# Optimization experiments

Hardware: AMD Instinct MI355X
Metric: run time of the kernel (lower is better)

The kernel has to match this reference:

```python
import jax, jax.numpy as jnp
import numpy as np

N = 50000      # nodes
E = 800000     # edges
G = 512        # graphs in batch
F0 = 92        # orig atom feature len
F = 64         # atom_fea_len
NB = 41        # nbr_fea_len
H = 128        # h_fea_len
NCONV = 3
EPS = 1e-5


def setup_inputs() -> dict:
    key = jax.random.key(0)
    ks = jax.random.split(key, 16)
    s = 0.05
    inp = {
        "x": jax.random.normal(ks[0], (N, F0), jnp.float32),
        "edge_index": jax.random.randint(ks[1], (2, E), 0, N),
        "edge_attr": jax.random.normal(ks[2], (E, NB), jnp.float32),
        "batch": jnp.sort(jax.random.randint(ks[3], (N,), 0, G)),
        # embedding (only applied at the first conv, when x width == F0)
        "emb_W": jax.random.normal(ks[4], (F0, F), jnp.float32) * s,
        "emb_b": jnp.zeros((F,), jnp.float32),
        # per-conv-layer params, stacked on leading axis
        "bn1_g": jnp.ones((NCONV, F), jnp.float32),
        "bn1_b": jnp.zeros((NCONV, F), jnp.float32),
        "bn2_g": jnp.ones((NCONV, F), jnp.float32),
        "bn2_b": jnp.zeros((NCONV, F), jnp.float32),
        "lnf_W": jax.random.normal(ks[5], (NCONV, 2 * F + NB, F), jnp.float32) * s,
        "lnf_b": jnp.zeros((NCONV, F), jnp.float32),
        "lns_W": jax.random.normal(ks[6], (NCONV, 2 * F + NB, F), jnp.float32) * s,
        "lns_b": jnp.zeros((NCONV, F), jnp.float32),
        # readout MLP
        "fc1_W": jax.random.normal(ks[7], (F, H), jnp.float32) * s,
        "fc1_b": jnp.zeros((H,), jnp.float32),
        "out_W": jax.random.normal(ks[8], (H, 1), jnp.float32) * s,
        "out_b": jnp.zeros((1,), jnp.float32),
    }
    return inp


def _batchnorm(x, g, b):
    # training-mode BatchNorm1d: batch stats over node dim, biased variance
    mean = jnp.mean(x, axis=0)
    var = jnp.var(x, axis=0)
    return (x - mean) * jax.lax.rsqrt(var + EPS) * g + b


def _cgconv(x, edge_index, edge_attr, bn1_g, bn1_b, bn2_g, bn2_b, Wf, bf, Ws, bs):
    x = _batchnorm(x, bn1_g, bn1_b)
    # flow='target_to_source': x_i = x[edge_index[0]], x_j = x[edge_index[1]],
    # aggregation scatter-adds messages to edge_index[0]
    src, dst = edge_index[0], edge_index[1]
    z = jnp.concatenate([x[src], x[dst], edge_attr], axis=-1)   # [E, 2F+NB]
    m = jax.nn.sigmoid(z @ Wf + bf) * jax.nn.softplus(z @ Ws + bs)
    agg = jax.ops.segment_sum(m, src, num_segments=x.shape[0])  # [N, F]
    out = _batchnorm(agg, bn2_g, bn2_b) + x
    return jax.nn.softplus(out)


def reference(x, edge_index, edge_attr, batch, emb_W, emb_b,
              bn1_g, bn1_b, bn2_g, bn2_b, lnf_W, lnf_b, lns_W, lns_b,
              fc1_W, fc1_b, out_W, out_b):
    h = x @ emb_W + emb_b  # first conv applies embedding (x width == F0)
    for i in range(NCONV):
        h = _cgconv(h, edge_index, edge_attr,
                    bn1_g[i], bn1_b[i], bn2_g[i], bn2_b[i],
                    lnf_W[i], lnf_b[i], lns_W[i], lns_b[i])
    # global mean pool per graph
    sums = jax.ops.segment_sum(h, batch, num_segments=G)
    cnts = jax.ops.segment_sum(jnp.ones((h.shape[0], 1), h.dtype), batch, num_segments=G)
    crys = sums / jnp.maximum(cnts, 1.0)                         # [G, F]
    crys = jax.nn.softplus(jax.nn.softplus(crys) @ fc1_W + fc1_b)
    return crys @ out_W + out_b                                  # [G, 1]
```

## Files before the change

### kernel.cpp

```cpp
#include <hip/hip_runtime.h>
#include <hip/hip_bf16.h>

#define NN 50000
#define NE 800000
#define NG 512
#define F0 92
#define FF 64
#define NB 41
#define HH 128
#define NBLK_SCAN 196
#define NBATCH (NE / 64)
#define WBSZ (2 * 8 * 64 * 8)

typedef __attribute__((ext_vector_type(4))) float f32x4;
typedef __attribute__((ext_vector_type(8))) short bf16x8;

__device__ __forceinline__ float softplusf(float x) {
    return fmaxf(x, 0.f) + __logf(1.f + __expf(-fabsf(x)));
}
__device__ __forceinline__ float sigmoidf(float x) {
    return __fdividef(1.f, 1.f + __expf(-x));
}
__device__ __forceinline__ ushort f2bf(float v) {
    __hip_bfloat16 b = __float2bfloat16(v);
    return *reinterpret_cast<ushort*>(&b);
}


__global__ __launch_bounds__(256) void hist_kernel(const int* __restrict__ ei,
                                                   int* __restrict__ cnt)
{
    for (int e = blockIdx.x * 256 + threadIdx.x; e < NE; e += gridDim.x * 256)
        atomicAdd(&cnt[ei[e]], 1);
}

__global__ __launch_bounds__(256) void scan1_kernel(const int* __restrict__ cnt,
                                                    int* __restrict__ bsum)
{
    __shared__ int sd[256];
    const int t = threadIdx.x;
    const int idx = blockIdx.x * 256 + t;
    sd[t] = (idx < NN) ? cnt[idx] : 0;
    __syncthreads();
    for (int s = 128; s > 0; s >>= 1) {
        if (t < s) sd[t] += sd[t + s];
        __syncthreads();
    }
    if (t == 0) bsum[blockIdx.x] = sd[0];
}

__global__ __launch_bounds__(256) void scan2_kernel(int* __restrict__ bsum)
{
    __shared__ int sd[256];
    const int t = threadIdx.x;
    const int v = (t < NBLK_SCAN) ? bsum[t] : 0;
    sd[t] = v;
    __syncthreads();
    for (int off = 1; off < 256; off <<= 1) {
        int a = (t >= off) ? sd[t - off] : 0;
        __syncthreads();
        sd[t] += a;
        __syncthreads();
    }
    if (t < NBLK_SCAN) bsum[t] = sd[t] - v;
}

__global__ __launch_bounds__(256) void scan3_kernel(const int* __restrict__ cnt,
                                                    const int* __restrict__ bsum,
                                                    int* __restrict__ cursor)
{
    __shared__ int sd[256];
    const int t = threadIdx.x;
    const int idx = blockIdx.x * 256 + t;
    const int v = (idx < NN) ? cnt[idx] : 0;
    sd[t] = v;
    __syncthreads();
    for (int off = 1; off < 256; off <<= 1) {
        int a = (t >= off) ? sd[t - off] : 0;
        __syncthreads();
        sd[t] += a;
        __syncthreads();
    }
    if (idx < NN) cursor[idx] = bsum[blockIdx.x] + sd[t] - v;
}

__global__ __launch_bounds__(256) void scatter_kernel(const int* __restrict__ ei,
                                                      int* __restrict__ cursor,
                                                      int4* __restrict__ esd)
{
    for (int e = blockIdx.x * 256 + threadIdx.x; e < NE; e += gridDim.x * 256) {
        const int s = ei[e];
        const int d = ei[NE + e];
        const int pos = atomicAdd(&cursor[s], 1);
        esd[pos] = make_int4(e, s, d, 0);
    }
}

__global__ __launch_bounds__(256) void pack_kernel(const float* __restrict__ ea,
                                                   const int4* __restrict__ esd,
                                                   ushort* __restrict__ eaP)
{
    const int pos = blockIdx.x * 256 + threadIdx.x;
    if (pos >= NE) return;
    const int e = esd[pos].x;
    const float* row = ea + (size_t)e * NB;
    const int gg = pos >> 4, rw = pos & 15;
#pragma unroll
    for (int t2 = 0; t2 < 2; ++t2)
#pragma unroll
        for (int lg = 0; lg < 4; ++lg) {
            ushort buf[8] __attribute__((aligned(16)));
#pragma unroll
            for (int j = 0; j < 8; ++j) {
                const int k = t2 * 32 + lg * 8 + j;
                buf[j] = (k < NB) ? f2bf(row[k]) : (ushort)0;
            }
            *(int4*)&eaP[(((size_t)gg * 2 + t2) * 64 + lg * 16 + rw) * 8] =
                *(const int4*)buf;
        }
}

__global__ __launch_bounds__(256) void prep_kernel(
    const float* __restrict__ lnfW, const float* __restrict__ lnsW,
    ushort* __restrict__ wB)
{
    const int total = 3 * WBSZ;
    for (int idx = blockIdx.x * 256 + threadIdx.x; idx < total; idx += gridDim.x * 256) {
        const int j = idx & 7;
        const int lane = (idx >> 3) & 63;
        const int nt = (idx >> 9) & 7;
        const int t2 = (idx >> 12) & 1;
        const int i = idx >> 13;
        const int k = t2 * 32 + (lane >> 4) * 8 + j;
        const int col = (nt & 3) * 16 + (lane & 15);
        const float* W = (nt < 4 ? lnfW : lnsW) + (size_t)i * 169 * FF;
        wB[idx] = (k < NB) ? f2bf(W[(2 * FF + k) * FF + col]) : (ushort)0;
    }
}


__global__ __launch_bounds__(256) void emb_kernel(
    const float* __restrict__ x, const float* __restrict__ W,
    const float* __restrict__ bias, float* __restrict__ h,
    float* __restrict__ stats0)
{
    __shared__ float sx[4][F0];
    __shared__ float sdr[2][4][FF];
    const int lane = threadIdx.x & 63;
    const int w = threadIdx.x >> 6;
    float wr[F0];
#pragma unroll
    for (int k = 0; k < F0; ++k) wr[k] = W[k * FF + lane];
    const float bv = bias[lane];
    float s = 0.f, s2 = 0.f;
    const int nit = NN / 4;
    for (int it = blockIdx.x; it < nit; it += gridDim.x) {
        const int n = it * 4 + w;
        if (lane < 46) {
            sx[w][lane * 2]     = x[n * F0 + lane * 2];
            sx[w][lane * 2 + 1] = x[n * F0 + lane * 2 + 1];
        }
        float acc = bv;
#pragma unroll
        for (int k4 = 0; k4 < F0 / 4; ++k4) {
            float4 q = *(const float4*)&sx[w][k4 * 4];
            acc = fmaf(q.x, wr[k4 * 4 + 0], acc);
            acc = fmaf(q.y, wr[k4 * 4 + 1], acc);
            acc = fmaf(q.z, wr[k4 * 4 + 2], acc);
            acc = fmaf(q.w, wr[k4 * 4 + 3], acc);
        }
        h[n * FF + lane] = acc;
        s += acc;
        s2 = fmaf(acc, acc, s2);
    }
    sdr[0][w][lane] = s;
    sdr[1][w][lane] = s2;
    __syncthreads();
    if (threadIdx.x < FF) {
        const int f = threadIdx.x;
        atomicAdd(&stats0[f],      sdr[0][0][f] + sdr[0][1][f] + sdr[0][2][f] + sdr[0][3][f]);
        atomicAdd(&stats0[FF + f], sdr[1][0][f] + sdr[1][1][f] + sdr[1][2][f] + sdr[1][3][f]);
    }
}

__global__ __launch_bounds__(256) void stats_kernel(
    const float* __restrict__ src, float* __restrict__ stats)
{
    __shared__ float sd[2][4][FF];
    const int f = threadIdx.x & 63;
    const int r = threadIdx.x >> 6;
    float s = 0.f, s2 = 0.f;
    for (int n = blockIdx.x * 4 + r; n < NN; n += gridDim.x * 4) {
        float v = src[n * FF + f];
        s += v;
        s2 = fmaf(v, v, s2);
    }
    sd[0][r][f] = s;
    sd[1][r][f] = s2;
    __syncthreads();
    if (threadIdx.x < FF) {
        atomicAdd(&stats[f],      sd[0][0][f] + sd[0][1][f] + sd[0][2][f] + sd[0][3][f]);
        atomicAdd(&stats[FF + f], sd[1][0][f] + sd[1][1][f] + sd[1][2][f] + sd[1][3][f]);
    }
}

__global__ __launch_bounds__(256) void node_kernel(
    const float* __restrict__ h, const float* __restrict__ stats,
    const float* __restrict__ gbn, const float* __restrict__ bbn,
    const float* __restrict__ Wf, const float* __restrict__ Ws,
    const float* __restrict__ bf, const float* __restrict__ bs,
    float* __restrict__ xn, float* __restrict__ pS, float* __restrict__ pD)
{
    __shared__ float sx[4][FF];
    const int lane = threadIdx.x & 63;
    const int w = threadIdx.x >> 6;
    const float* W = (w < 2) ? Wf : Ws;
    const int rowbase = (w & 1) * FF;
    float wr[FF];
#pragma unroll
    for (int k = 0; k < FF; ++k) wr[k] = W[(rowbase + k) * FF + lane];
    const float inv = 1.f / (float)NN;
    const float mean = stats[lane] * inv;
    const float var = stats[FF + lane] * inv - mean * mean;
    const float A = rsqrtf(var + 1e-5f) * gbn[lane];
    const float B = fmaf(-mean, A, bbn[lane]);
    float bias = 0.f;
    if (w == 0) bias = bf[lane];
    if (w == 2) bias = bs[lane];
    float* outp = ((w & 1) ? pD : pS) + ((w >> 1) & 1);
    for (int n = blockIdx.x; n < NN; n += gridDim.x) {
        const float xv = fmaf(h[n * FF + lane], A, B);
        if (w == 0) xn[n * FF + lane] = xv;
        sx[w][lane] = xv;
        float acc = bias;
#pragma unroll
        for (int k4 = 0; k4 < FF / 4; ++k4) {
            float4 q = *(const float4*)&sx[w][k4 * 4];
            acc = fmaf(q.x, wr[k4 * 4 + 0], acc);
            acc = fmaf(q.y, wr[k4 * 4 + 1], acc);
            acc = fmaf(q.z, wr[k4 * 4 + 2], acc);
            acc = fmaf(q.w, wr[k4 * 4 + 3], acc);
        }
        outp[(size_t)n * 128 + 2 * lane] = acc;
    }
}

__global__ __launch_bounds__(256) __attribute__((amdgpu_waves_per_eu(4, 4)))
void edge_kernel(const ushort* __restrict__ eaP, const int4* __restrict__ esd,
                 const ushort* __restrict__ wB,
                 const float* __restrict__ pS, const float* __restrict__ pD,
                 float* __restrict__ agg)
{
    __shared__ ushort wlds[WBSZ];
    __shared__ float  mld[4][64 * 17 + 4];
    __shared__ int    sld[4][64];
    __shared__ int    dld[4][64];
    const int t = threadIdx.x, lane = t & 63, w = t >> 6;
    for (int i = t; i < WBSZ / 8; i += 256)
        ((int4*)wlds)[i] = ((const int4*)wB)[i];
    __syncthreads();
    const int le = lane >> 4, lf = lane & 15;
    const int nw = (gridDim.x * 256) >> 6;
    const int gw = (blockIdx.x * 256 + t) >> 6;

    for (int b = gw; b < NBATCH; b += nw) {
        const int pos = b * 64 + lane;
        const int4 rec = esd[pos];
        sld[w][lane] = rec.y;
        dld[w][lane] = rec.z;
        bf16x8 af[4][2];
#pragma unroll
        for (int g = 0; g < 4; ++g)
#pragma unroll
            for (int t2 = 0; t2 < 2; ++t2)
                af[g][t2] = *(const bf16x8*)&eaP[(((size_t)(b * 4 + g) * 2 + t2) * 64 + lane) * 8];

#pragma unroll
        for (int p = 0; p < 4; ++p) {
            const bf16x8 bG0 = *(const bf16x8*)&wlds[((0 * 8 + p) * 64 + lane) * 8];
            const bf16x8 bG1 = *(const bf16x8*)&wlds[((1 * 8 + p) * 64 + lane) * 8];
            const bf16x8 bC0 = *(const bf16x8*)&wlds[((0 * 8 + p + 4) * 64 + lane) * 8];
            const bf16x8 bC1 = *(const bf16x8*)&wlds[((1 * 8 + p + 4) * 64 + lane) * 8];
            const int f = p * 16 + lf;
#pragma unroll
            for (int g = 0; g < 4; ++g) {
                f32x4 aG = {0.f, 0.f, 0.f, 0.f}, aC = {0.f, 0.f, 0.f, 0.f};
                aG = __builtin_amdgcn_mfma_f32_16x16x32_bf16(af[g][0], bG0, aG, 0, 0, 0);
                aG = __builtin_amdgcn_mfma_f32_16x16x32_bf16(af[g][1], bG1, aG, 0, 0, 0);
                aC = __builtin_amdgcn_mfma_f32_16x16x32_bf16(af[g][0], bC0, aC, 0, 0, 0);
                aC = __builtin_amdgcn_mfma_f32_16x16x32_bf16(af[g][1], bC1, aC, 0, 0, 0);
                const int eb = g * 16 + le * 4;
#pragma unroll
                for (int r = 0; r < 4; ++r) {
                    const int eidx = eb + r;
                    const int sv = sld[w][eidx];
                    const int dv = dld[w][eidx];
                    const float2 s2 = *(const float2*)(pS + (size_t)sv * 128 + 2 * f);
                    const float2 d2 = *(const float2*)(pD + (size_t)dv * 128 + 2 * f);
                    mld[w][eidx * 17 + lf] =
                        sigmoidf(aG[r] + s2.x + d2.x) * softplusf(aC[r] + s2.y + d2.y);
                }
            }
            const int f0 = p * 16;
            for (int s = 0; s < 16; ++s) {
                const int eidx = s * 4 + le;
                float v = mld[w][eidx * 17 + lf];
                const int sA = sld[w][eidx];
                const int sB = (le <= 2) ? sld[w][eidx + 1] : -1;
                const int sC = (le <= 1) ? sld[w][eidx + 2] : -1;
                const float t1 = __shfl_down(v, 16, 64);
                if (sB == sA) v += t1;
                const float t2v = __shfl_down(v, 32, 64);
                if (sC == sA) v += t2v;
                const bool head = (le == 0) || (sld[w][eidx - 1] != sA);
                if (head) unsafeAtomicAdd(&agg[(size_t)sA * FF + f0 + lf], v);
            }
        }
    }
}

__global__ __launch_bounds__(256) void update_kernel(
    const float* __restrict__ agg, const float* __restrict__ xn,
    const float* __restrict__ stats,
    const float* __restrict__ gbn, const float* __restrict__ bbn,
    float* __restrict__ h, const int* __restrict__ batch,
    float* __restrict__ pool, float* __restrict__ pcnt,
    float* __restrict__ statsNext, const int do_pool)
{
    __shared__ float sdr[2][4][FF];
    const int myf = threadIdx.x & 63;
    const float inv = 1.f / (float)NN;
    const float mean = stats[myf] * inv;
    const float var = stats[FF + myf] * inv - mean * mean;
    const float A = rsqrtf(var + 1e-5f) * gbn[myf];
    const float B = fmaf(-mean, A, bbn[myf]);
    float s = 0.f, s2 = 0.f;
    const int total = NN * FF;
    for (int idx = blockIdx.x * blockDim.x + threadIdx.x; idx < total;
         idx += gridDim.x * blockDim.x) {
        const int n = idx >> 6;
        const float v = softplusf(fmaf(agg[idx], A, B) + xn[idx]);
        if (do_pool) {
            const int g = batch[n];
            unsafeAtomicAdd(&pool[g * FF + myf], v);
            if (myf == 0) unsafeAtomicAdd(&pcnt[g], 1.f);
        } else {
            h[idx] = v;
            s += v;
            s2 = fmaf(v, v, s2);
        }
    }
    if (!do_pool) {
        const int r = threadIdx.x >> 6;
        sdr[0][r][myf] = s;
        sdr[1][r][myf] = s2;
        __syncthreads();
        if (threadIdx.x < FF) {
            atomicAdd(&statsNext[myf],      sdr[0][0][myf] + sdr[0][1][myf] + sdr[0][2][myf] + sdr[0][3][myf]);
            atomicAdd(&statsNext[FF + myf], sdr[1][0][myf] + sdr[1][1][myf] + sdr[1][2][myf] + sdr[1][3][myf]);
        }
    }
}

__global__ __launch_bounds__(128) void readout_kernel(
    const float* __restrict__ pool, const float* __restrict__ pcnt,
    const float* __restrict__ fc1W, const float* __restrict__ fc1b,
    const float* __restrict__ outW, const float* __restrict__ outb,
    float* __restrict__ out)
{
    __shared__ float sp[FF];
    __shared__ float red[2];
    const int g = blockIdx.x;
    const int t = threadIdx.x;
    if (t < FF) {
        const float c = fmaxf(pcnt[g], 1.f);
        sp[t] = softplusf(pool[g * FF + t] / c);
    }
    __syncthreads();
    float a = fc1b[t];
#pragma unroll
    for (int k = 0; k < FF; ++k) a = fmaf(sp[k], fc1W[k * HH + t], a);
    float o = softplusf(a) * outW[t];
#pragma unroll
    for (int off = 32; off > 0; off >>= 1) o += __shfl_down(o, off, 64);
    if ((t & 63) == 0) red[t >> 6] = o;
    __syncthreads();
    if (t == 0) out[g] = red[0] + red[1] + outb[0];
}

extern "C" void kernel_launch(void* const* d_in, const int* in_sizes, int n_in,
                              void* d_out, int out_size, void* d_ws, size_t ws_size,
                              hipStream_t stream)
{
    const float* x     = (const float*)d_in[0];
    const int*   ei    = (const int*)  d_in[1];
    const float* ea    = (const float*)d_in[2];
    const int*   batch = (const int*)  d_in[3];
    const float* embW  = (const float*)d_in[4];
    const float* embb  = (const float*)d_in[5];
    const float* bn1g  = (const float*)d_in[6];
    const float* bn1b  = (const float*)d_in[7];
    const float* bn2g  = (const float*)d_in[8];
    const float* bn2b  = (const float*)d_in[9];
    const float* lnfW  = (const float*)d_in[10];
    const float* lnfb  = (const float*)d_in[11];
    const float* lnsW  = (const float*)d_in[12];
    const float* lnsb  = (const float*)d_in[13];
    const float* fc1W  = (const float*)d_in[14];
    const float* fc1b  = (const float*)d_in[15];
    const float* outW  = (const float*)d_in[16];
    const float* outb  = (const float*)d_in[17];

    float* ws      = (float*)d_ws;
    float* h       = ws;
    float* xn      = h   + (size_t)NN * FF;
    float* pS      = xn  + (size_t)NN * FF;
    float* pD      = pS  + (size_t)NN * 128;
    float* agg     = pD  + (size_t)NN * 128;
    float* pool    = agg + (size_t)NN * FF;
    float* pcnt    = pool + (size_t)NG * FF;
    float* statsB1 = pcnt + NG;
    float* statsB2 = statsB1 + 3 * 256;
    int*   cnt     = (int*)(statsB2 + 3 * 256);
    int*   cursor  = cnt + NN;
    int*   bsum    = cursor + NN;
    int4*  esd     = (int4*)(bsum + 256);
    ushort* wB     = (ushort*)(esd + NE);
    ushort* eaP    = wB + 3 * WBSZ;

    hipMemsetAsync(cnt, 0, NN * sizeof(int), stream);
    hipMemsetAsync(pool, 0, (NG * FF + NG + 6 * 256) * sizeof(float), stream);

    hist_kernel<<<2048, 256, 0, stream>>>(ei, cnt);
    scan1_kernel<<<NBLK_SCAN, 256, 0, stream>>>(cnt, bsum);
    scan2_kernel<<<1, 256, 0, stream>>>(bsum);
    scan3_kernel<<<NBLK_SCAN, 256, 0, stream>>>(cnt, bsum, cursor);
    scatter_kernel<<<2048, 256, 0, stream>>>(ei, cursor, esd);
    pack_kernel<<<(NE + 255) / 256, 256, 0, stream>>>(ea, esd, eaP);
    prep_kernel<<<96, 256, 0, stream>>>(lnfW, lnsW, wB);
    emb_kernel<<<2048, 256, 0, stream>>>(x, embW, embb, h, statsB1);

    for (int i = 0; i < 3; ++i) {
        const float* Wf  = lnfW + (size_t)i * 169 * FF;
        const float* Wsp = lnsW + (size_t)i * 169 * FF;
        float* s1 = statsB1 + (size_t)i * 256;
        float* s2 = statsB2 + (size_t)i * 256;
        node_kernel<<<2048, 256, 0, stream>>>(h, s1, bn1g + i * FF, bn1b + i * FF,
                                              Wf, Wsp, lnfb + i * FF, lnsb + i * FF,
                                              xn, pS, pD);
        hipMemsetAsync(agg, 0, (size_t)NN * FF * sizeof(float), stream);
        edge_kernel<<<1024, 256, 0, stream>>>(eaP, esd, wB + (size_t)i * WBSZ,
                                              pS, pD, agg);
        stats_kernel<<<1024, 256, 0, stream>>>(agg, s2);
        update_kernel<<<2048, 256, 0, stream>>>(agg, xn, s2, bn2g + i * FF, bn2b + i * FF,
                                                h, batch, pool, pcnt,
                                                statsB1 + (size_t)(i + 1 < 3 ? i + 1 : 0) * 256,
                                                (i == 2) ? 1 : 0);
    }
    readout_kernel<<<NG, HH, 0, stream>>>(pool, pcnt, fc1W, fc1b, outW, outb, (float*)d_out);
}
```

Baseline: 971.4 us.

## Pack edge attributes in original order and gather rows by edge id in edge kernel

The pack kernel no longer follows the sorted edge permutation. It stages contiguous edge_attr rows in shared memory with coalesced loads and writes row-major bf16 rows of 64 elements. The edge kernel now shuffles each edge's original id and gathers its two 16-byte fragments from that packed row. This removes the pack kernel's random row reads. In exchange, the edge kernel does scattered 16-byte loads three times, once per conv layer, instead of fully coalesced streaming loads.

```diff
diff --git a/kernel.cpp b/kernel.cpp
--- a/kernel.cpp
+++ b/kernel.cpp
@@ -11,6 +11,7 @@
 #define NBLK_SCAN 196
 #define NBATCH (NE / 64)
 #define WBSZ (2 * 8 * 64 * 8)
+#define PACK_EB 128
 
 typedef __attribute__((ext_vector_type(4))) float f32x4;
 typedef __attribute__((ext_vector_type(8))) short bf16x8;
@@ -96,28 +97,24 @@
     }
 }
 
-__global__ __launch_bounds__(256) void pack_kernel(const float* __restrict__ ea,
-                                                   const int4* __restrict__ esd,
+__global__ __launch_bounds__(128) void pack_kernel(const float* __restrict__ ea,
                                                    ushort* __restrict__ eaP)
 {
-    const int pos = blockIdx.x * 256 + threadIdx.x;
-    if (pos >= NE) return;
-    const int e = esd[pos].x;
-    const float* row = ea + (size_t)e * NB;
-    const int gg = pos >> 4, rw = pos & 15;
-#pragma unroll
-    for (int t2 = 0; t2 < 2; ++t2)
-#pragma unroll
-        for (int lg = 0; lg < 4; ++lg) {
-            ushort buf[8] __attribute__((aligned(16)));
-#pragma unroll
-            for (int j = 0; j < 8; ++j) {
-                const int k = t2 * 32 + lg * 8 + j;
-                buf[j] = (k < NB) ? f2bf(row[k]) : (ushort)0;
-            }
-            *(int4*)&eaP[(((size_t)gg * 2 + t2) * 64 + lg * 16 + rw) * 8] =
-                *(const int4*)buf;
-        }
+    __shared__ float rowbuf[PACK_EB * NB];
+    const int t = threadIdx.x;
+    const size_t base = (size_t)blockIdx.x * PACK_EB;
+    const float* src = ea + base * NB;
+    for (int i = t; i < PACK_EB * NB; i += 128) rowbuf[i] = src[i];
+    __syncthreads();
+    uint* out = (uint*)eaP + base * 32;
+#pragma unroll
+    for (int i = 0; i < 32; ++i) {
+        const int idx = i * 128 + t;
+        const int e = idx >> 5, k2 = (idx & 31) * 2;
+        const float v0 = (k2 < NB) ? rowbuf[e * NB + k2] : 0.f;
+        const float v1 = (k2 + 1 < NB) ? rowbuf[e * NB + k2 + 1] : 0.f;
+        out[idx] = (uint)f2bf(v0) | ((uint)f2bf(v1) << 16);
+    }
 }
 
 __global__ __launch_bounds__(256) void prep_kernel(
@@ -270,10 +267,11 @@
         dld[w][lane] = rec.z;
         bf16x8 af[4][2];
 #pragma unroll
-        for (int g = 0; g < 4; ++g)
-#pragma unroll
-            for (int t2 = 0; t2 < 2; ++t2)
-                af[g][t2] = *(const bf16x8*)&eaP[(((size_t)(b * 4 + g) * 2 + t2) * 64 + lane) * 8];
+        for (int g = 0; g < 4; ++g) {
+            const int eg = __shfl(rec.x, g * 16 + lf, 64);
+            af[g][0] = *(const bf16x8*)&eaP[(size_t)eg * 64 + le * 8];
+            af[g][1] = *(const bf16x8*)&eaP[(size_t)eg * 64 + 32 + le * 8];
+        }
 
 #pragma unroll
         for (int p = 0; p < 4; ++p) {
@@ -436,7 +434,7 @@
     scan2_kernel<<<1, 256, 0, stream>>>(bsum);
     scan3_kernel<<<NBLK_SCAN, 256, 0, stream>>>(cnt, bsum, cursor);
     scatter_kernel<<<2048, 256, 0, stream>>>(ei, cursor, esd);
-    pack_kernel<<<(NE + 255) / 256, 256, 0, stream>>>(ea, esd, eaP);
+    pack_kernel<<<NE / PACK_EB, 128, 0, stream>>>(ea, eaP);
     prep_kernel<<<96, 256, 0, stream>>>(lnfW, lnsW, wB);
     emb_kernel<<<2048, 256, 0, stream>>>(x, embW, embb, h, statsB1);
 
```

Result: no change. 975.5 us (+0.4%).
